# Kernel tuning notes

Measured on AMD Instinct MI355X. Metric: run time of the kernel, lower is better.

The kernel has to match this reference:

```python
import jax, jax.numpy as jnp
import numpy as np

N_NODES = 500_000
N_EDGES = 16_000_000


def setup_inputs() -> dict:
    key = jax.random.key(0)
    ks = jax.random.split(key, 12)
    s = 0.3  # weight scale (glorot-ish for tiny dims)
    return {
        "x": jax.random.normal(ks[0], (N_NODES, 8), jnp.float32),
        "edge_index": jax.random.randint(ks[1], (2, N_EDGES), 0, N_NODES, jnp.int32),
        # GCNConv layers store weight as [out, in] (applied as x @ W.T) and a bias [out]
        "W1": jax.random.normal(ks[2], (4, 8), jnp.float32) * s,
        "b1": jnp.zeros((4,), jnp.float32),
        "W2": jax.random.normal(ks[3], (4, 4), jnp.float32) * s,
        "b2": jnp.zeros((4,), jnp.float32),
        "W3": jax.random.normal(ks[4], (2, 4), jnp.float32) * s,
        "b3": jnp.zeros((2,), jnp.float32),
        "W4": jax.random.normal(ks[5], (2, 2), jnp.float32) * s,
        "b4": jnp.zeros((2,), jnp.float32),
        "Wc": jax.random.normal(ks[6], (112, 2), jnp.float32) * s,
        "bc": jnp.zeros((112,), jnp.float32),
    }


def reference(x, edge_index, W1, b1, W2, b2, W3, b3, W4, b4, Wc, bc):
    n = x.shape[0]
    src, dst = edge_index[0], edge_index[1]

    # PyG GCNConv normalization with self-loops: deg includes the self-loop (+1),
    # norm(e) = deg^{-1/2}[src] * deg^{-1/2}[dst]; self-loop norm = deg^{-1}[i].
    deg = jax.ops.segment_sum(jnp.ones_like(dst, jnp.float32), dst, num_segments=n) + 1.0
    dinv = jax.lax.rsqrt(deg)
    norm = dinv[src] * dinv[dst]          # [E]
    self_norm = dinv * dinv               # [N]

    def conv(h, W, b):
        h = h @ W.T                                                    # [N, out]
        agg = jax.ops.segment_sum(norm[:, None] * h[src], dst, num_segments=n)
        return agg + self_norm[:, None] * h + b                        # self-loop + bias

    h = jax.nn.relu(conv(x, W1, b1))
    h = jnp.tanh(conv(h, W2, b2))
    h = jax.nn.relu(conv(h, W3, b3))
    h = jnp.tanh(conv(h, W4, b4))
    out = h @ Wc.T + bc
    return (out, h)
```

## Files before the change

### kernel.cpp

```cpp
#include <hip/hip_runtime.h>
#include <math.h>


constexpr int NN = 500000;
constexpr int NE = 16000000;

constexpr int BSH  = 9;
constexpr int BNODES = 1 << BSH;
constexpr int NBK  = (NN + BNODES - 1) / BNODES;
constexpr int BCAP = 18432;
constexpr int ECHUNK = 16384;
constexpr int NBA = (NE + ECHUNK - 1) / ECHUNK;

__device__ __forceinline__ void aadd(float* p, float v) {
    unsafeAtomicAdd(p, v);
}


__global__ __launch_bounds__(256) void k_tinit(int* __restrict__ tail) {
    int i = blockIdx.x * 256 + threadIdx.x;
    if (i < NBK) tail[i] = i * BCAP;
}

__global__ __launch_bounds__(256) void k_binA(const int* __restrict__ src,
                                              const int* __restrict__ dst,
                                              int* __restrict__ tail,
                                              unsigned* __restrict__ bins) {
    __shared__ int cnt[NBK];
    __shared__ int bbase[NBK];
    const int t = threadIdx.x;
    for (int k = t; k < NBK; k += 256) cnt[k] = 0;
    __syncthreads();

    const long e0 = (long)blockIdx.x * ECHUNK;
    const int ne = (int)min((long)ECHUNK, (long)NE - e0);
    const int g0 = (int)(e0 >> 2);
    const int ng = ne >> 2;

    for (int g = t; g < ng; g += 256) {
        int4 d = ((const int4*)dst)[g0 + g];
        atomicAdd(&cnt[d.x >> BSH], 1);
        atomicAdd(&cnt[d.y >> BSH], 1);
        atomicAdd(&cnt[d.z >> BSH], 1);
        atomicAdd(&cnt[d.w >> BSH], 1);
    }
    __syncthreads();
    for (int k = t; k < NBK; k += 256) {
        int c = cnt[k];
        bbase[k] = c ? atomicAdd(&tail[k], c) : 0;
        cnt[k] = 0;
    }
    __syncthreads();
    for (int g = t; g < ng; g += 256) {
        int4 d = ((const int4*)dst)[g0 + g];
        int4 s = ((const int4*)src)[g0 + g];
        int b, r, idx;
        b = d.x >> BSH; r = atomicAdd(&cnt[b], 1); idx = bbase[b] + r;
        if (idx < (b + 1) * BCAP)
            bins[idx] = ((unsigned)(d.x & (BNODES - 1)) << 19) | (unsigned)s.x;
        b = d.y >> BSH; r = atomicAdd(&cnt[b], 1); idx = bbase[b] + r;
        if (idx < (b + 1) * BCAP)
            bins[idx] = ((unsigned)(d.y & (BNODES - 1)) << 19) | (unsigned)s.y;
        b = d.z >> BSH; r = atomicAdd(&cnt[b], 1); idx = bbase[b] + r;
        if (idx < (b + 1) * BCAP)
            bins[idx] = ((unsigned)(d.z & (BNODES - 1)) << 19) | (unsigned)s.z;
        b = d.w >> BSH; r = atomicAdd(&cnt[b], 1); idx = bbase[b] + r;
        if (idx < (b + 1) * BCAP)
            bins[idx] = ((unsigned)(d.w & (BNODES - 1)) << 19) | (unsigned)s.w;
    }
}

__global__ __launch_bounds__(256) void k_rebinC(const unsigned* __restrict__ bins0,
                                                const int* __restrict__ tail,
                                                unsigned* __restrict__ bins1,
                                                int* __restrict__ astart,
                                                int* __restrict__ cnt) {
    __shared__ int c1[BNODES];
    __shared__ int wb[BNODES];
    __shared__ int c2[BNODES];
    const int b = blockIdx.x;
    const int t = threadIdx.x;
    c1[t] = 0; c1[t + 256] = 0;
    c2[t] = 0; c2[t + 256] = 0;
    __syncthreads();
    const int base = b * BCAP;
    const int n = min(tail[b] - base, BCAP);
    const unsigned* e0 = bins0 + base;
    for (int j = t; j < n; j += 256) atomicAdd(&c1[e0[j] >> 19], 1);
    __syncthreads();
    if (t == 0) {
        int o = 0;
        for (int r = 0; r < BNODES; ++r) {
            wb[r] = o;
            o = (o + c1[r] + 3) & ~3;
        }
    }
    __syncthreads();
    const int nb = b << BSH;
    cnt[nb + t] = c1[t];
    cnt[nb + t + 256] = c1[t + 256];
    astart[nb + t] = base + wb[t];
    astart[nb + t + 256] = base + wb[t + 256];
    for (int j = t; j < n; j += 256) {
        unsigned v = e0[j];
        int l = v >> 19;
        int k = atomicAdd(&c2[l], 1);
        int idx = wb[l] + k;
        if (idx < BCAP) bins1[base + idx] = v & 0x7FFFFu;
    }
}

__global__ __launch_bounds__(256) void k_t1n(const float* __restrict__ x,
                                             const float* __restrict__ W,
                                             const int* __restrict__ cnt,
                                             float* __restrict__ dinv,
                                             float* __restrict__ hp) {
    int i = blockIdx.x * 256 + threadIdx.x;
    if (i >= NN) return;
    float4 x0 = ((const float4*)x)[2 * i];
    float4 x1 = ((const float4*)x)[2 * i + 1];
    float xi[8] = {x0.x, x0.y, x0.z, x0.w, x1.x, x1.y, x1.z, x1.w};
    float di = rsqrtf((float)cnt[i] + 1.0f);
    dinv[i] = di;
    float o[4];
#pragma unroll
    for (int j = 0; j < 4; ++j) {
        float s = 0.f;
#pragma unroll
        for (int k = 0; k < 8; ++k) s = fmaf(xi[k], W[j * 8 + k], s);
        o[j] = di * s;
    }
    ((float4*)hp)[i] = make_float4(o[0], o[1], o[2], o[3]);
}

template <int IND, int OUTD, bool RELU>
__global__ __launch_bounds__(256) void g_csr(const int* __restrict__ astart,
                                             const int* __restrict__ cnt,
                                             const unsigned* __restrict__ bins,
                                             const float* __restrict__ dinv,
                                             const float* __restrict__ hin,
                                             const float* __restrict__ bp,
                                             const float* __restrict__ Wn,
                                             float* __restrict__ hout) {
    int i = blockIdx.x * 256 + threadIdx.x;
    if (i >= NN) return;
    const int cn = cnt[i];
    const uint4* rp = (const uint4*)bins + (astart[i] >> 2);
    float acc[IND];
    if constexpr (IND == 4) {
        float4 sv = ((const float4*)hin)[i];
        acc[0] = sv.x; acc[1] = sv.y; acc[2] = sv.z; acc[3] = sv.w;
    } else {
        float2 sv = ((const float2*)hin)[i];
        acc[0] = sv.x; acc[1] = sv.y;
    }
    const int full = cn >> 2, rem = cn & 3;
    int j = 0;
    for (; j + 2 <= full; j += 2) {
        uint4 a = rp[j], c = rp[j + 1];
        if constexpr (IND == 4) {
            float4 h0 = ((const float4*)hin)[a.x];
            float4 h1 = ((const float4*)hin)[a.y];
            float4 h2 = ((const float4*)hin)[a.z];
            float4 h3 = ((const float4*)hin)[a.w];
            float4 h4 = ((const float4*)hin)[c.x];
            float4 h5 = ((const float4*)hin)[c.y];
            float4 h6 = ((const float4*)hin)[c.z];
            float4 h7 = ((const float4*)hin)[c.w];
            acc[0] += ((h0.x + h1.x) + (h2.x + h3.x)) + ((h4.x + h5.x) + (h6.x + h7.x));
            acc[1] += ((h0.y + h1.y) + (h2.y + h3.y)) + ((h4.y + h5.y) + (h6.y + h7.y));
            acc[2] += ((h0.z + h1.z) + (h2.z + h3.z)) + ((h4.z + h5.z) + (h6.z + h7.z));
            acc[3] += ((h0.w + h1.w) + (h2.w + h3.w)) + ((h4.w + h5.w) + (h6.w + h7.w));
        } else {
            float2 h0 = ((const float2*)hin)[a.x];
            float2 h1 = ((const float2*)hin)[a.y];
            float2 h2 = ((const float2*)hin)[a.z];
            float2 h3 = ((const float2*)hin)[a.w];
            float2 h4 = ((const float2*)hin)[c.x];
            float2 h5 = ((const float2*)hin)[c.y];
            float2 h6 = ((const float2*)hin)[c.z];
            float2 h7 = ((const float2*)hin)[c.w];
            acc[0] += ((h0.x + h1.x) + (h2.x + h3.x)) + ((h4.x + h5.x) + (h6.x + h7.x));
            acc[1] += ((h0.y + h1.y) + (h2.y + h3.y)) + ((h4.y + h5.y) + (h6.y + h7.y));
        }
    }
    if (j < full) {
        uint4 a = rp[j];
        if constexpr (IND == 4) {
            float4 h0 = ((const float4*)hin)[a.x];
            float4 h1 = ((const float4*)hin)[a.y];
            float4 h2 = ((const float4*)hin)[a.z];
            float4 h3 = ((const float4*)hin)[a.w];
            acc[0] += (h0.x + h1.x) + (h2.x + h3.x);
            acc[1] += (h0.y + h1.y) + (h2.y + h3.y);
            acc[2] += (h0.z + h1.z) + (h2.z + h3.z);
            acc[3] += (h0.w + h1.w) + (h2.w + h3.w);
        } else {
            float2 h0 = ((const float2*)hin)[a.x];
            float2 h1 = ((const float2*)hin)[a.y];
            float2 h2 = ((const float2*)hin)[a.z];
            float2 h3 = ((const float2*)hin)[a.w];
            acc[0] += (h0.x + h1.x) + (h2.x + h3.x);
            acc[1] += (h0.y + h1.y) + (h2.y + h3.y);
        }
    }
    if (rem) {
        uint4 a = rp[full];
        unsigned s1 = rem > 1 ? a.y : a.x;
        unsigned s2 = rem > 2 ? a.z : a.x;
        float w1 = rem > 1 ? 1.f : 0.f;
        float w2 = rem > 2 ? 1.f : 0.f;
        if constexpr (IND == 4) {
            float4 h0 = ((const float4*)hin)[a.x];
            float4 h1 = ((const float4*)hin)[s1];
            float4 h2 = ((const float4*)hin)[s2];
            acc[0] += h0.x + w1 * h1.x + w2 * h2.x;
            acc[1] += h0.y + w1 * h1.y + w2 * h2.y;
            acc[2] += h0.z + w1 * h1.z + w2 * h2.z;
            acc[3] += h0.w + w1 * h1.w + w2 * h2.w;
        } else {
            float2 h0 = ((const float2*)hin)[a.x];
            float2 h1 = ((const float2*)hin)[s1];
            float2 h2 = ((const float2*)hin)[s2];
            acc[0] += h0.x + w1 * h1.x + w2 * h2.x;
            acc[1] += h0.y + w1 * h1.y + w2 * h2.y;
        }
    }
    const float di = dinv[i];
    float h[IND];
#pragma unroll
    for (int k = 0; k < IND; ++k) {
        float v = di * acc[k] + bp[k];
        h[k] = RELU ? fmaxf(v, 0.f) : tanhf(v);
    }
    float o[OUTD];
#pragma unroll
    for (int q = 0; q < OUTD; ++q) {
        float s = 0.f;
#pragma unroll
        for (int k = 0; k < IND; ++k) s = fmaf(h[k], Wn[q * IND + k], s);
        o[q] = di * s;
    }
    if constexpr (OUTD == 4)
        ((float4*)hout)[i] = make_float4(o[0], o[1], o[2], o[3]);
    else
        ((float2*)hout)[i] = make_float2(o[0], o[1]);
}

__global__ __launch_bounds__(256) void g_csrF(const int* __restrict__ astart,
                                              const int* __restrict__ cnt,
                                              const unsigned* __restrict__ bins,
                                              const float* __restrict__ dinv,
                                              const float* __restrict__ hin,
                                              const float* __restrict__ b4,
                                              float* __restrict__ hout2) {
    int i = blockIdx.x * 256 + threadIdx.x;
    if (i >= NN) return;
    const int cn = cnt[i];
    const uint4* rp = (const uint4*)bins + (astart[i] >> 2);
    float2 sv = ((const float2*)hin)[i];
    float a0 = sv.x, a1 = sv.y;
    const int full = cn >> 2, rem = cn & 3;
    int j = 0;
    for (; j + 2 <= full; j += 2) {
        uint4 a = rp[j], c = rp[j + 1];
        float2 h0 = ((const float2*)hin)[a.x];
        float2 h1 = ((const float2*)hin)[a.y];
        float2 h2 = ((const float2*)hin)[a.z];
        float2 h3 = ((const float2*)hin)[a.w];
        float2 h4 = ((const float2*)hin)[c.x];
        float2 h5 = ((const float2*)hin)[c.y];
        float2 h6 = ((const float2*)hin)[c.z];
        float2 h7 = ((const float2*)hin)[c.w];
        a0 += ((h0.x + h1.x) + (h2.x + h3.x)) + ((h4.x + h5.x) + (h6.x + h7.x));
        a1 += ((h0.y + h1.y) + (h2.y + h3.y)) + ((h4.y + h5.y) + (h6.y + h7.y));
    }
    if (j < full) {
        uint4 a = rp[j];
        float2 h0 = ((const float2*)hin)[a.x];
        float2 h1 = ((const float2*)hin)[a.y];
        float2 h2 = ((const float2*)hin)[a.z];
        float2 h3 = ((const float2*)hin)[a.w];
        a0 += (h0.x + h1.x) + (h2.x + h3.x);
        a1 += (h0.y + h1.y) + (h2.y + h3.y);
    }
    if (rem) {
        uint4 a = rp[full];
        unsigned s1 = rem > 1 ? a.y : a.x;
        unsigned s2 = rem > 2 ? a.z : a.x;
        float w1 = rem > 1 ? 1.f : 0.f;
        float w2 = rem > 2 ? 1.f : 0.f;
        float2 h0 = ((const float2*)hin)[a.x];
        float2 h1 = ((const float2*)hin)[s1];
        float2 h2 = ((const float2*)hin)[s2];
        a0 += h0.x + w1 * h1.x + w2 * h2.x;
        a1 += h0.y + w1 * h1.y + w2 * h2.y;
    }
    const float di = dinv[i];
    float h0 = tanhf(di * a0 + b4[0]);
    float h1 = tanhf(di * a1 + b4[1]);
    ((float2*)hout2)[i] = make_float2(h0, h1);
}

__global__ __launch_bounds__(256) void k_f2(const float* __restrict__ h,
                                            const float* __restrict__ Wc,
                                            const float* __restrict__ bc,
                                            float* __restrict__ out) {
    int t = blockIdx.x * 256 + threadIdx.x;
    if (t >= NN * 28) return;
    int n = t / 28;
    int r = t - n * 28;
    int k = 4 * r;
    float2 hv = ((const float2*)h)[n];
    float4 o;
    o.x = fmaf(hv.y, Wc[2 * k + 1], fmaf(hv.x, Wc[2 * k + 0], bc[k + 0]));
    o.y = fmaf(hv.y, Wc[2 * k + 3], fmaf(hv.x, Wc[2 * k + 2], bc[k + 1]));
    o.z = fmaf(hv.y, Wc[2 * k + 5], fmaf(hv.x, Wc[2 * k + 4], bc[k + 2]));
    o.w = fmaf(hv.y, Wc[2 * k + 7], fmaf(hv.x, Wc[2 * k + 6], bc[k + 3]));
    ((float4*)out)[(size_t)n * 28 + r] = o;
}


__global__ __launch_bounds__(256) void k_init_deg(float* __restrict__ deg) {
    int i = blockIdx.x * 256 + threadIdx.x;
    if (i < NN) deg[i] = 1.0f;
}

__global__ __launch_bounds__(256) void k_count(const int* __restrict__ dst,
                                               float* __restrict__ deg) {
    int t = blockIdx.x * 256 + threadIdx.x;
    int4 d = ((const int4*)dst)[t];
    aadd(deg + d.x, 1.0f); aadd(deg + d.y, 1.0f);
    aadd(deg + d.z, 1.0f); aadd(deg + d.w, 1.0f);
}

__global__ __launch_bounds__(256) void k_dinv(float* __restrict__ deg) {
    int i = blockIdx.x * 256 + threadIdx.x;
    if (i < NN) deg[i] = 1.0f / sqrtf(deg[i]);
}

__global__ __launch_bounds__(256) void k_t1(const float* __restrict__ x,
                                            const float* __restrict__ W,
                                            const float* __restrict__ dinv,
                                            float* __restrict__ hp,
                                            float* __restrict__ ac) {
    int i = blockIdx.x * 256 + threadIdx.x;
    if (i >= NN) return;
    float4 x0 = ((const float4*)x)[2 * i];
    float4 x1 = ((const float4*)x)[2 * i + 1];
    float xi[8] = {x0.x, x0.y, x0.z, x0.w, x1.x, x1.y, x1.z, x1.w};
    float di = dinv[i];
    float o[4];
#pragma unroll
    for (int j = 0; j < 4; ++j) {
        float s = 0.f;
#pragma unroll
        for (int k = 0; k < 8; ++k) s = fmaf(xi[k], W[j * 8 + k], s);
        o[j] = di * s;
    }
    ((float4*)hp)[i] = make_float4(o[0], o[1], o[2], o[3]);
    ((float4*)ac)[i] = make_float4(0.f, 0.f, 0.f, 0.f);
}

__global__ __launch_bounds__(256) void k_s4(const int* __restrict__ src,
                                            const int* __restrict__ dst,
                                            const float* __restrict__ hp,
                                            float* __restrict__ ac) {
    int t = blockIdx.x * 256 + threadIdx.x;
    int4 s = ((const int4*)src)[t];
    int4 d = ((const int4*)dst)[t];
    float4 h;
    h = ((const float4*)hp)[s.x];
    aadd(ac + 4 * d.x + 0, h.x); aadd(ac + 4 * d.x + 1, h.y);
    aadd(ac + 4 * d.x + 2, h.z); aadd(ac + 4 * d.x + 3, h.w);
    h = ((const float4*)hp)[s.y];
    aadd(ac + 4 * d.y + 0, h.x); aadd(ac + 4 * d.y + 1, h.y);
    aadd(ac + 4 * d.y + 2, h.z); aadd(ac + 4 * d.y + 3, h.w);
    h = ((const float4*)hp)[s.z];
    aadd(ac + 4 * d.z + 0, h.x); aadd(ac + 4 * d.z + 1, h.y);
    aadd(ac + 4 * d.z + 2, h.z); aadd(ac + 4 * d.z + 3, h.w);
    h = ((const float4*)hp)[s.w];
    aadd(ac + 4 * d.w + 0, h.x); aadd(ac + 4 * d.w + 1, h.y);
    aadd(ac + 4 * d.w + 2, h.z); aadd(ac + 4 * d.w + 3, h.w);
}

__global__ __launch_bounds__(256) void k_s2(const int* __restrict__ src,
                                            const int* __restrict__ dst,
                                            const float* __restrict__ hp,
                                            float* __restrict__ ac) {
    int t = blockIdx.x * 256 + threadIdx.x;
    int4 s = ((const int4*)src)[t];
    int4 d = ((const int4*)dst)[t];
    float2 h;
    h = ((const float2*)hp)[s.x];
    aadd(ac + 2 * d.x + 0, h.x); aadd(ac + 2 * d.x + 1, h.y);
    h = ((const float2*)hp)[s.y];
    aadd(ac + 2 * d.y + 0, h.x); aadd(ac + 2 * d.y + 1, h.y);
    h = ((const float2*)hp)[s.z];
    aadd(ac + 2 * d.z + 0, h.x); aadd(ac + 2 * d.z + 1, h.y);
    h = ((const float2*)hp)[s.w];
    aadd(ac + 2 * d.w + 0, h.x); aadd(ac + 2 * d.w + 1, h.y);
}

template <bool RELU>
__global__ __launch_bounds__(256) void k_t44(const float* __restrict__ dinv,
                                             float* __restrict__ hp,
                                             float* __restrict__ ac,
                                             const float* __restrict__ bprev,
                                             const float* __restrict__ Wn) {
    int i = blockIdx.x * 256 + threadIdx.x;
    if (i >= NN) return;
    float di = dinv[i];
    float4 hv = ((const float4*)hp)[i];
    float4 av = ((const float4*)ac)[i];
    float h[4];
    h[0] = di * (av.x + hv.x) + bprev[0];
    h[1] = di * (av.y + hv.y) + bprev[1];
    h[2] = di * (av.z + hv.z) + bprev[2];
    h[3] = di * (av.w + hv.w) + bprev[3];
#pragma unroll
    for (int k = 0; k < 4; ++k) h[k] = RELU ? fmaxf(h[k], 0.f) : tanhf(h[k]);
    float o[4];
#pragma unroll
    for (int j = 0; j < 4; ++j) {
        float s = 0.f;
#pragma unroll
        for (int k = 0; k < 4; ++k) s = fmaf(h[k], Wn[j * 4 + k], s);
        o[j] = di * s;
    }
    ((float4*)hp)[i] = make_float4(o[0], o[1], o[2], o[3]);
    ((float4*)ac)[i] = make_float4(0.f, 0.f, 0.f, 0.f);
}

__global__ __launch_bounds__(256) void k_t42(const float* __restrict__ dinv,
                                             const float* __restrict__ hp4,
                                             const float* __restrict__ ac4,
                                             const float* __restrict__ bprev,
                                             const float* __restrict__ Wn,
                                             float* __restrict__ hp2,
                                             float* __restrict__ ac2) {
    int i = blockIdx.x * 256 + threadIdx.x;
    if (i >= NN) return;
    float di = dinv[i];
    float4 hv = ((const float4*)hp4)[i];
    float4 av = ((const float4*)ac4)[i];
    float h[4];
    h[0] = tanhf(di * (av.x + hv.x) + bprev[0]);
    h[1] = tanhf(di * (av.y + hv.y) + bprev[1]);
    h[2] = tanhf(di * (av.z + hv.z) + bprev[2]);
    h[3] = tanhf(di * (av.w + hv.w) + bprev[3]);
    float o0 = 0.f, o1 = 0.f;
#pragma unroll
    for (int k = 0; k < 4; ++k) {
        o0 = fmaf(h[k], Wn[k], o0);
        o1 = fmaf(h[k], Wn[4 + k], o1);
    }
    ((float2*)hp2)[i] = make_float2(di * o0, di * o1);
    ((float2*)ac2)[i] = make_float2(0.f, 0.f);
}

__global__ __launch_bounds__(256) void k_t22(const float* __restrict__ dinv,
                                             float* __restrict__ hp,
                                             float* __restrict__ ac,
                                             const float* __restrict__ bprev,
                                             const float* __restrict__ Wn) {
    int i = blockIdx.x * 256 + threadIdx.x;
    if (i >= NN) return;
    float di = dinv[i];
    float2 hv = ((const float2*)hp)[i];
    float2 av = ((const float2*)ac)[i];
    float h0 = fmaxf(di * (av.x + hv.x) + bprev[0], 0.f);
    float h1 = fmaxf(di * (av.y + hv.y) + bprev[1], 0.f);
    float o0 = fmaf(h1, Wn[1], h0 * Wn[0]);
    float o1 = fmaf(h1, Wn[3], h0 * Wn[2]);
    ((float2*)hp)[i] = make_float2(di * o0, di * o1);
    ((float2*)ac)[i] = make_float2(di * 0.f, di * 0.f);
}

__global__ __launch_bounds__(256) void k_f1(const float* __restrict__ dinv,
                                            const float* __restrict__ hp,
                                            float* __restrict__ ac,
                                            const float* __restrict__ b4,
                                            float* __restrict__ hout) {
    int i = blockIdx.x * 256 + threadIdx.x;
    if (i >= NN) return;
    float di = dinv[i];
    float2 hv = ((const float2*)hp)[i];
    float2 av = ((const float2*)ac)[i];
    float h0 = tanhf(di * (av.x + hv.x) + b4[0]);
    float h1 = tanhf(di * (av.y + hv.y) + b4[1]);
    ((float2*)hout)[i] = make_float2(h0, h1);
    ((float2*)ac)[i] = make_float2(h0, h1);
}


extern "C" void kernel_launch(void* const* d_in, const int* in_sizes, int n_in,
                              void* d_out, int out_size, void* d_ws, size_t ws_size,
                              hipStream_t stream) {
    const float* x   = (const float*)d_in[0];
    const int*   ei  = (const int*)d_in[1];
    const int*   src = ei;
    const int*   dst = ei + NE;
    const float* W1 = (const float*)d_in[2];
    const float* b1 = (const float*)d_in[3];
    const float* W2 = (const float*)d_in[4];
    const float* b2 = (const float*)d_in[5];
    const float* W3 = (const float*)d_in[6];
    const float* b3 = (const float*)d_in[7];
    const float* W4 = (const float*)d_in[8];
    const float* b4 = (const float*)d_in[9];
    const float* Wc = (const float*)d_in[10];
    const float* bc = (const float*)d_in[11];
    float* out = (float*)d_out;
    float* hN2 = out + (size_t)112 * NN;

    const int NB_N  = (NN + 255) / 256;
    const int NB_E4 = NE / 4 / 256;
    const int NB_F2 = (NN * 28 + 255) / 256;

    const size_t binsz = (size_t)NBK * BCAP;
    const size_t nodesz = (size_t)NBK << BSH;
    const size_t need_new =
        ((size_t)13 * NN + 1024 + 2 * nodesz + 2 * binsz) * 4;

    if (ws_size >= need_new) {
        float* ws   = (float*)d_ws;
        float* dinv = ws;
        float* hpA  = ws + (size_t)NN;
        float* hpB  = ws + (size_t)5 * NN;
        float* h2A  = ws + (size_t)9 * NN;
        float* h2B  = ws + (size_t)11 * NN;
        int*   tail = (int*)(ws + (size_t)13 * NN);
        int*   cntA = tail + 1024;
        int*   astart = cntA + nodesz;
        unsigned* bins0 = (unsigned*)(astart + nodesz);
        unsigned* bins1 = bins0 + binsz;

        k_tinit<<<(NBK + 255) / 256, 256, 0, stream>>>(tail);
        k_binA<<<NBA, 256, 0, stream>>>(src, dst, tail, bins0);
        k_rebinC<<<NBK, 256, 0, stream>>>(bins0, tail, bins1, astart, cntA);
        k_t1n<<<NB_N, 256, 0, stream>>>(x, W1, cntA, dinv, hpA);
        g_csr<4, 4, true ><<<NB_N, 256, 0, stream>>>(astart, cntA, bins1, dinv, hpA, b1, W2, hpB);
        g_csr<4, 2, false><<<NB_N, 256, 0, stream>>>(astart, cntA, bins1, dinv, hpB, b2, W3, h2A);
        g_csr<2, 2, true ><<<NB_N, 256, 0, stream>>>(astart, cntA, bins1, dinv, h2A, b3, W4, h2B);
        g_csrF<<<NB_N, 256, 0, stream>>>(astart, cntA, bins1, dinv, h2B, b4, hN2);
        k_f2<<<NB_F2, 256, 0, stream>>>(hN2, Wc, bc, out);
    } else {
        float* ws   = (float*)d_ws;
        float* dinv = ws;
        float* hp4  = ws + (size_t)NN;
        float* ac4  = ws + (size_t)5 * NN;
        float* hp2  = ws + (size_t)9 * NN;
        float* ac2  = ws + (size_t)11 * NN;

        k_init_deg<<<NB_N, 256, 0, stream>>>(dinv);
        k_count<<<NB_E4, 256, 0, stream>>>(dst, dinv);
        k_dinv<<<NB_N, 256, 0, stream>>>(dinv);
        k_t1<<<NB_N, 256, 0, stream>>>(x, W1, dinv, hp4, ac4);
        k_s4<<<NB_E4, 256, 0, stream>>>(src, dst, hp4, ac4);
        k_t44<true><<<NB_N, 256, 0, stream>>>(dinv, hp4, ac4, b1, W2);
        k_s4<<<NB_E4, 256, 0, stream>>>(src, dst, hp4, ac4);
        k_t42<<<NB_N, 256, 0, stream>>>(dinv, hp4, ac4, b2, W3, hp2, ac2);
        k_s2<<<NB_E4, 256, 0, stream>>>(src, dst, hp2, ac2);
        k_t22<<<NB_N, 256, 0, stream>>>(dinv, hp2, ac2, b3, W4);
        k_s2<<<NB_E4, 256, 0, stream>>>(src, dst, hp2, ac2);
        k_f1<<<NB_N, 256, 0, stream>>>(dinv, hp2, ac2, b4, hN2);
        k_f2<<<NB_F2, 256, 0, stream>>>(ac2, Wc, bc, out);
    }
}
```

Measured before the change: 1.462 ms.

## Stage binned edges in LDS to coalesce global writes in binning and rebin

Adds new binning and rebinning kernels that first sort each edge chunk locally in shared memory, using a prefix scan over bin counts, and then write it to global memory contiguously. The old kernels scattered each edge straight to a global bin slot. The rebin kernel also builds the per-node CSR segment in LDS and copies it out with uint4 stores. This trades a large dynamic shared-memory footprint (96KB and 72KB per block), which lowers occupancy, for better-coalesced global writes.

```diff
diff --git a/kernel.cpp b/kernel.cpp
--- a/kernel.cpp
+++ b/kernel.cpp
@@ -11,6 +11,8 @@
 constexpr int BCAP = 18432;
 constexpr int ECHUNK = 16384;
 constexpr int NBA = (NE + ECHUNK - 1) / ECHUNK;
+constexpr int DYN_BINB  = ECHUNK * 4 + ECHUNK * 2;
+constexpr int DYN_REBIN = BCAP * 4;
 
 __device__ __forceinline__ void aadd(float* p, float v) {
     unsafeAtomicAdd(p, v);
@@ -20,6 +22,89 @@
 __global__ __launch_bounds__(256) void k_tinit(int* __restrict__ tail) {
     int i = blockIdx.x * 256 + threadIdx.x;
     if (i < NBK) tail[i] = i * BCAP;
+}
+
+__global__ __launch_bounds__(256) void k_binB(const int* __restrict__ src,
+                                              const int* __restrict__ dst,
+                                              int* __restrict__ tail,
+                                              unsigned* __restrict__ bins) {
+    extern __shared__ unsigned dynbuf[];
+    unsigned* chunk = dynbuf;
+    unsigned short* bid = (unsigned short*)(dynbuf + ECHUNK);
+    __shared__ int c1[NBK];
+    __shared__ int lofs[NBK];
+    __shared__ int dlt[NBK];
+    __shared__ int wsum[4];
+    const int t = threadIdx.x;
+    for (int k = t; k < NBK; k += 256) c1[k] = 0;
+    __syncthreads();
+
+    const long e0l = (long)blockIdx.x * ECHUNK;
+    const int ne = (int)min((long)ECHUNK, (long)NE - e0l);
+    const int g0 = (int)(e0l >> 2);
+    const int ng = ne >> 2;
+
+    for (int g = t; g < ng; g += 256) {
+        int4 d = ((const int4*)dst)[g0 + g];
+        atomicAdd(&c1[d.x >> BSH], 1);
+        atomicAdd(&c1[d.y >> BSH], 1);
+        atomicAdd(&c1[d.z >> BSH], 1);
+        atomicAdd(&c1[d.w >> BSH], 1);
+    }
+    __syncthreads();
+    int b0 = 4 * t;
+    int v0 = b0 + 0 < NBK ? c1[b0 + 0] : 0;
+    int v1 = b0 + 1 < NBK ? c1[b0 + 1] : 0;
+    int v2 = b0 + 2 < NBK ? c1[b0 + 2] : 0;
+    int v3 = b0 + 3 < NBK ? c1[b0 + 3] : 0;
+    int loc = v0 + v1 + v2 + v3, inc = loc;
+#pragma unroll
+    for (int d = 1; d < 64; d <<= 1) {
+        int u = __shfl_up(inc, d);
+        if ((t & 63) >= d) inc += u;
+    }
+    if ((t & 63) == 63) wsum[t >> 6] = inc;
+    __syncthreads();
+    int wo = 0;
+    for (int k = 0; k < (t >> 6); ++k) wo += wsum[k];
+    int ex = wo + inc - loc;
+    if (b0 + 0 < NBK) lofs[b0 + 0] = ex;
+    if (b0 + 1 < NBK) lofs[b0 + 1] = ex + v0;
+    if (b0 + 2 < NBK) lofs[b0 + 2] = ex + v0 + v1;
+    if (b0 + 3 < NBK) lofs[b0 + 3] = ex + v0 + v1 + v2;
+    __syncthreads();
+    for (int k = t; k < NBK; k += 256) {
+        int c = c1[k];
+        if (c) {
+            int gb = atomicAdd(&tail[k], c);
+            dlt[k] = gb - lofs[k];
+        }
+        c1[k] = 0;
+    }
+    __syncthreads();
+    for (int g = t; g < ng; g += 256) {
+        int4 d = ((const int4*)dst)[g0 + g];
+        int4 s = ((const int4*)src)[g0 + g];
+        int bb, r, p;
+        bb = d.x >> BSH; r = atomicAdd(&c1[bb], 1); p = lofs[bb] + r;
+        chunk[p] = ((unsigned)(d.x & (BNODES - 1)) << 19) | (unsigned)s.x;
+        bid[p] = (unsigned short)bb;
+        bb = d.y >> BSH; r = atomicAdd(&c1[bb], 1); p = lofs[bb] + r;
+        chunk[p] = ((unsigned)(d.y & (BNODES - 1)) << 19) | (unsigned)s.y;
+        bid[p] = (unsigned short)bb;
+        bb = d.z >> BSH; r = atomicAdd(&c1[bb], 1); p = lofs[bb] + r;
+        chunk[p] = ((unsigned)(d.z & (BNODES - 1)) << 19) | (unsigned)s.z;
+        bid[p] = (unsigned short)bb;
+        bb = d.w >> BSH; r = atomicAdd(&c1[bb], 1); p = lofs[bb] + r;
+        chunk[p] = ((unsigned)(d.w & (BNODES - 1)) << 19) | (unsigned)s.w;
+        bid[p] = (unsigned short)bb;
+    }
+    __syncthreads();
+    for (int p = t; p < ne; p += 256) {
+        int bb = bid[p];
+        int idx = p + dlt[bb];
+        if (idx < (bb + 1) * BCAP) bins[idx] = chunk[p];
+    }
 }
 
 __global__ __launch_bounds__(256) void k_binA(const int* __restrict__ src,
@@ -31,12 +116,10 @@
     const int t = threadIdx.x;
     for (int k = t; k < NBK; k += 256) cnt[k] = 0;
     __syncthreads();
-
     const long e0 = (long)blockIdx.x * ECHUNK;
     const int ne = (int)min((long)ECHUNK, (long)NE - e0);
     const int g0 = (int)(e0 >> 2);
     const int ng = ne >> 2;
-
     for (int g = t; g < ng; g += 256) {
         int4 d = ((const int4*)dst)[g0 + g];
         atomicAdd(&cnt[d.x >> BSH], 1);
@@ -68,6 +151,63 @@
         if (idx < (b + 1) * BCAP)
             bins[idx] = ((unsigned)(d.w & (BNODES - 1)) << 19) | (unsigned)s.w;
     }
+}
+
+__global__ __launch_bounds__(256) void k_rebinD(const unsigned* __restrict__ bins0,
+                                                const int* __restrict__ tail,
+                                                unsigned* __restrict__ bins1,
+                                                int* __restrict__ astart,
+                                                int* __restrict__ cnt) {
+    extern __shared__ unsigned sb[];
+    __shared__ int c1[BNODES];
+    __shared__ int wb[BNODES];
+    __shared__ int c2[BNODES];
+    __shared__ int wsum[4];
+    const int b = blockIdx.x;
+    const int t = threadIdx.x;
+    c1[t] = 0; c1[t + 256] = 0;
+    c2[t] = 0; c2[t + 256] = 0;
+    __syncthreads();
+    const int base = b * BCAP;
+    const int n = min(tail[b] - base, BCAP);
+    const unsigned* e0 = bins0 + base;
+    for (int j = t; j < n; j += 256) atomicAdd(&c1[e0[j] >> 19], 1);
+    __syncthreads();
+    int a0 = c1[2 * t], a1 = c1[2 * t + 1];
+    int p0 = (a0 + 3) & ~3, p1 = (a1 + 3) & ~3;
+    int loc = p0 + p1, inc = loc;
+#pragma unroll
+    for (int d = 1; d < 64; d <<= 1) {
+        int u = __shfl_up(inc, d);
+        if ((t & 63) >= d) inc += u;
+    }
+    if ((t & 63) == 63) wsum[t >> 6] = inc;
+    __syncthreads();
+    int wo = 0;
+    for (int k = 0; k < (t >> 6); ++k) wo += wsum[k];
+    int ex = wo + inc - loc;
+    wb[2 * t] = ex;
+    wb[2 * t + 1] = ex + p0;
+    const int nb = b << BSH;
+    cnt[nb + 2 * t] = a0;
+    cnt[nb + 2 * t + 1] = a1;
+    astart[nb + 2 * t] = base + ex;
+    astart[nb + 2 * t + 1] = base + ex + p0;
+    __syncthreads();
+    for (int j = t; j < n; j += 256) {
+        unsigned v = e0[j];
+        int l = v >> 19;
+        int r = atomicAdd(&c2[l], 1);
+        int p = wb[l] + r;
+        if (p < BCAP) sb[p] = v & 0x7FFFFu;
+    }
+    __syncthreads();
+    int span = wb[BNODES - 1] + ((c1[BNODES - 1] + 3) & ~3);
+    if (span > BCAP) span = BCAP;
+    const int nq = span >> 2;
+    uint4* d4 = (uint4*)(bins1 + base);
+    const uint4* s4 = (const uint4*)sb;
+    for (int q = t; q < nq; q += 256) d4[q] = s4[q];
 }
 
 __global__ __launch_bounds__(256) void k_rebinC(const unsigned* __restrict__ bins0,
@@ -518,6 +658,17 @@
     const int NB_E4 = NE / 4 / 256;
     const int NB_F2 = (NN * 28 + 255) / 256;
 
+    static int dyn_ok = -1;
+    if (dyn_ok < 0) {
+        hipError_t e1 = hipFuncSetAttribute(
+            reinterpret_cast<const void*>(k_binB),
+            hipFuncAttributeMaxDynamicSharedMemorySize, DYN_BINB);
+        hipError_t e2 = hipFuncSetAttribute(
+            reinterpret_cast<const void*>(k_rebinD),
+            hipFuncAttributeMaxDynamicSharedMemorySize, DYN_REBIN);
+        dyn_ok = (e1 == hipSuccess && e2 == hipSuccess) ? 1 : 0;
+    }
+
     const size_t binsz = (size_t)NBK * BCAP;
     const size_t nodesz = (size_t)NBK << BSH;
     const size_t need_new =
@@ -537,8 +688,13 @@
         unsigned* bins1 = bins0 + binsz;
 
         k_tinit<<<(NBK + 255) / 256, 256, 0, stream>>>(tail);
-        k_binA<<<NBA, 256, 0, stream>>>(src, dst, tail, bins0);
-        k_rebinC<<<NBK, 256, 0, stream>>>(bins0, tail, bins1, astart, cntA);
+        if (dyn_ok) {
+            k_binB<<<NBA, 256, DYN_BINB, stream>>>(src, dst, tail, bins0);
+            k_rebinD<<<NBK, 256, DYN_REBIN, stream>>>(bins0, tail, bins1, astart, cntA);
+        } else {
+            k_binA<<<NBA, 256, 0, stream>>>(src, dst, tail, bins0);
+            k_rebinC<<<NBK, 256, 0, stream>>>(bins0, tail, bins1, astart, cntA);
+        }
         k_t1n<<<NB_N, 256, 0, stream>>>(x, W1, cntA, dinv, hpA);
         g_csr<4, 4, true ><<<NB_N, 256, 0, stream>>>(astart, cntA, bins1, dinv, hpA, b1, W2, hpB);
         g_csr<4, 2, false><<<NB_N, 256, 0, stream>>>(astart, cntA, bins1, dinv, hpB, b2, W3, h2A);
```

Result: faster. 1.174 ms (-19.7%).
